# Performance work log

Measured on AMD Instinct MI355X. Metric: run time of the kernel, lower is better.

Reference implementation:

```python
import jax, jax.numpy as jnp
import numpy as np

DIM = 512
NUM_HEADS = 1
WS = 16
B, H, W = 2, WS * WS, 1


def _rel_pos_index(ws):
    # matches Attention.calculate_relative_position_index (no Swin offset -> negatives)
    coords = np.stack(np.meshgrid(np.arange(ws), np.arange(ws), indexing='ij'), 0).reshape(2, -1)
    rel = coords[:, :, None] - coords[:, None, :]          # [2, ws^2, ws^2]
    return rel.transpose(1, 2, 0).sum(-1)                  # [ws^2, ws^2] in [-(2ws-2), 2ws-2]

_NTAB = (2 * WS - 1) ** 2
# torch fancy indexing wraps negative indices; emulate with mod (values are in (-NTAB, NTAB))
_RPI = np.mod(_rel_pos_index(WS), _NTAB).reshape(-1)       # [ws^4]


def setup_inputs() -> dict:
    key = jax.random.key(0)
    ks = jax.random.split(key, 6)
    x = jax.random.normal(ks[0], (B, DIM, H, W), dtype=jnp.float32)
    qkv_w = jax.random.normal(ks[1], (3 * DIM, DIM), dtype=jnp.float32) * (DIM ** -0.5)
    qkv_b = jax.random.normal(ks[2], (3 * DIM,), dtype=jnp.float32) * 0.02
    proj_w = jax.random.normal(ks[3], (DIM, DIM), dtype=jnp.float32) * (DIM ** -0.5)
    proj_b = jax.random.normal(ks[4], (DIM,), dtype=jnp.float32) * 0.02
    rpb = jax.random.normal(ks[5], (_NTAB, NUM_HEADS), dtype=jnp.float32) * 0.02
    return {"x": x, "qkv_w": qkv_w, "qkv_b": qkv_b,
            "proj_w": proj_w, "proj_b": proj_b, "rpb": rpb}


def reference(x, qkv_w, qkv_b, proj_w, proj_b, rpb):
    b, c, h, w = x.shape                                   # [B, C, H, W=1]
    d = c // NUM_HEADS
    scale = d ** -0.5                                      # qk_scale=None -> (dim//nh)^-0.5
    # 1x1 conv == channel matmul
    qkv = jnp.einsum('bchw,oc->bohw', x, qkv_w) + qkv_b[None, :, None, None]
    qkv = qkv.reshape(b, 3, NUM_HEADS, d, h, w)
    q, k, v = qkv[:, 0], qkv[:, 1], qkv[:, 2]              # [B, nh, d, H, W]
    # matmul over last two dims: contracts W -> [B, nh, d, H, H]
    attn = jnp.einsum('bndhw,bndgw->bndhg', q, k) * scale
    idx = jnp.asarray(_RPI)
    bias = rpb[idx].reshape(h * w, h * w, -1).transpose(2, 0, 1)  # [nh, HW, HW] = [1, H, H]
    attn = jax.nn.softmax(attn + bias, axis=-1)
    out = jnp.einsum('bndhg,bndgw->bndhw', attn, v).sum(axis=1)   # sum over heads -> [B, d, H, W]
    out = jnp.einsum('bchw,oc->bohw', out, proj_w) + proj_b[None, :, None, None]
    return out
```

## Files before the change

### kernel.cpp

```cpp
#include <hip/hip_runtime.h>
#include <hip/hip_bf16.h>


#define TOK   256
#define KDIM  512
#define LOG2E 1.4426950408889634f
#define SCALE 0.04419417382415922f

#define EXP2(x) __builtin_amdgcn_exp2f(x)

struct K1Smem {
    union {
        float red[4][6][256];
        float brow[31][258];
    } u;
    float tab2[64];
    float ks_[2][TOK];
    float vs_[2][TOK];
    float qs_[2][TOK];
    float lpart[2][TOK], apart[2][TOK];
};

__global__ __launch_bounds__(256)
void qkv_attn(const float* __restrict__ x, const float* __restrict__ qkv_w,
              const float* __restrict__ qkv_b, const float* __restrict__ rpb,
              float* __restrict__ aout)
{
    __shared__ K1Smem sm;
    const int t    = threadIdx.x;
    const int d0   = blockIdx.x * 2;
    const int b    = blockIdx.y;
    const int w    = t >> 6;
    const int lane = t & 63;

    if (t < 61) {
        const int rel = t - 30;
        sm.tab2[t] = rpb[rel < 0 ? rel + 961 : rel] * LOG2E;
    }

    {
        const float* xb = x + (size_t)b * (KDIM * TOK);
        const int g0 = lane * 4;
        const float* wp[6];
        wp[0] = qkv_w + (size_t)(d0 + 0) * KDIM;
        wp[1] = qkv_w + (size_t)(d0 + 1) * KDIM;
        wp[2] = qkv_w + (size_t)(512 + d0 + 0) * KDIM;
        wp[3] = qkv_w + (size_t)(512 + d0 + 1) * KDIM;
        wp[4] = qkv_w + (size_t)(1024 + d0 + 0) * KDIM;
        wp[5] = qkv_w + (size_t)(1024 + d0 + 1) * KDIM;

        float acc[6][4];
#pragma unroll
        for (int e = 0; e < 6; ++e)
#pragma unroll
            for (int j = 0; j < 4; ++j) acc[e][j] = 0.f;

        const int cbeg = w * 128;
#pragma unroll 1
        for (int c = cbeg; c < cbeg + 128; c += 4) {
            float4 xv[4];
#pragma unroll
            for (int u = 0; u < 4; ++u)
                xv[u] = *(const float4*)(xb + (size_t)(c + u) * TOK + g0);
#pragma unroll
            for (int u = 0; u < 4; ++u) {
#pragma unroll
                for (int e = 0; e < 6; ++e) {
                    const float wv = wp[e][c + u];
                    acc[e][0] = fmaf(wv, xv[u].x, acc[e][0]);
                    acc[e][1] = fmaf(wv, xv[u].y, acc[e][1]);
                    acc[e][2] = fmaf(wv, xv[u].z, acc[e][2]);
                    acc[e][3] = fmaf(wv, xv[u].w, acc[e][3]);
                }
            }
        }
#pragma unroll
        for (int e = 0; e < 6; ++e)
            *(float4*)&sm.u.red[w][e][g0] = make_float4(acc[e][0], acc[e][1],
                                                        acc[e][2], acc[e][3]);
    }
    __syncthreads();

    {
#pragma unroll
        for (int e = 0; e < 6; ++e) {
            const float v = sm.u.red[0][e][t] + sm.u.red[1][e][t] +
                            sm.u.red[2][e][t] + sm.u.red[3][e][t];
            if (e < 2)      sm.qs_[e][t] = v + qkv_b[d0 + e];
            else if (e < 4) sm.ks_[e - 2][t] = (v + qkv_b[512 + d0 + e - 2]) *
                                               (SCALE * LOG2E);
            else            sm.vs_[e - 4][t] = v + qkv_b[1024 + d0 + e - 4];
        }
    }
    __syncthreads();

    {
        const int rg = ((t >> 4) & 15) + (t & 15);
#pragma unroll 1
        for (int it = 0; it < 31; ++it)
            sm.u.brow[it][t] = sm.tab2[it - rg + 30];
    }
    __syncthreads();

    const int dl  = w & 1;
    const int gh  = w >> 1;
    const int qi  = ((lane & 15) << 2) | (lane >> 4);
    const int h0  = qi * 4;
    const int rh0 = (qi >> 2) + 4 * (qi & 3);

    float q[4];
    {
        const float4 q4 = *(const float4*)&sm.qs_[dl][h0];
        q[0] = q4.x; q[1] = q4.y; q[2] = q4.z; q[3] = q4.w;
    }

    float l[4]  = {0.f, 0.f, 0.f, 0.f};
    float am[4] = {0.f, 0.f, 0.f, 0.f};
    const int pbeg = gh * 128;
#pragma unroll 2
    for (int p = pbeg; p < pbeg + 128; p += 4) {
        const float4 k4 = *(const float4*)&sm.ks_[dl][p];
        const float4 v4 = *(const float4*)&sm.vs_[dl][p];
#pragma unroll
        for (int r = 0; r < 4; ++r) {
            const float2 b01 = *(const float2*)&sm.u.brow[rh0 + r][p];
            const float2 b23 = *(const float2*)&sm.u.brow[rh0 + r][p + 2];
            float e;
            e = EXP2(fmaf(q[r], k4.x, b01.x)); l[r] += e; am[r] = fmaf(e, v4.x, am[r]);
            e = EXP2(fmaf(q[r], k4.y, b01.y)); l[r] += e; am[r] = fmaf(e, v4.y, am[r]);
            e = EXP2(fmaf(q[r], k4.z, b23.x)); l[r] += e; am[r] = fmaf(e, v4.z, am[r]);
            e = EXP2(fmaf(q[r], k4.w, b23.y)); l[r] += e; am[r] = fmaf(e, v4.w, am[r]);
        }
    }

    if (gh == 1) {
        *(float4*)&sm.lpart[dl][h0] = make_float4(l[0], l[1], l[2], l[3]);
        *(float4*)&sm.apart[dl][h0] = make_float4(am[0], am[1], am[2], am[3]);
    }
    __syncthreads();
    if (gh == 0) {
        const float4 lo = *(const float4*)&sm.lpart[dl][h0];
        const float4 ao = *(const float4*)&sm.apart[dl][h0];
        float4 o4;
        o4.x = (am[0] + ao.x) / (l[0] + lo.x);
        o4.y = (am[1] + ao.y) / (l[1] + lo.y);
        o4.z = (am[2] + ao.z) / (l[2] + lo.z);
        o4.w = (am[3] + ao.w) / (l[3] + lo.w);
        *(float4*)(aout + ((size_t)b * 512 + d0 + dl) * TOK + h0) = o4;
    }
}

__global__ __launch_bounds__(256)
void proj_fused(const float* __restrict__ aout, const float* __restrict__ proj_w,
                const float* __restrict__ proj_b, float* __restrict__ out)
{
    __shared__ float sred[4][4][256];
    const int t    = threadIdx.x;
    const int o0   = blockIdx.x * 4;
    const int b    = blockIdx.y;
    const int w    = t >> 6;
    const int g0   = (t & 63) * 4;

    const float* ab = aout + (size_t)b * (KDIM * TOK);
    const float* wp[4];
#pragma unroll
    for (int e = 0; e < 4; ++e)
        wp[e] = proj_w + (size_t)(o0 + e) * KDIM;

    float acc[4][4];
#pragma unroll
    for (int e = 0; e < 4; ++e)
#pragma unroll
        for (int j = 0; j < 4; ++j) acc[e][j] = 0.f;

    const int cbeg = w * 128;
#pragma unroll 1
    for (int c = cbeg; c < cbeg + 128; c += 4) {
        float4 av[4];
#pragma unroll
        for (int u = 0; u < 4; ++u)
            av[u] = *(const float4*)(ab + (size_t)(c + u) * TOK + g0);
#pragma unroll
        for (int u = 0; u < 4; ++u) {
#pragma unroll
            for (int e = 0; e < 4; ++e) {
                const float wv = wp[e][c + u];
                acc[e][0] = fmaf(wv, av[u].x, acc[e][0]);
                acc[e][1] = fmaf(wv, av[u].y, acc[e][1]);
                acc[e][2] = fmaf(wv, av[u].z, acc[e][2]);
                acc[e][3] = fmaf(wv, av[u].w, acc[e][3]);
            }
        }
    }
#pragma unroll
    for (int e = 0; e < 4; ++e)
        *(float4*)&sred[w][e][g0] = make_float4(acc[e][0], acc[e][1],
                                                acc[e][2], acc[e][3]);
    __syncthreads();

#pragma unroll
    for (int e = 0; e < 4; ++e) {
        const float v = sred[0][e][t] + sred[1][e][t] +
                        sred[2][e][t] + sred[3][e][t] + proj_b[o0 + e];
        out[((size_t)b * 512 + o0 + e) * TOK + t] = v;
    }
}

extern "C" void kernel_launch(void* const* d_in, const int* in_sizes, int n_in,
                              void* d_out, int out_size, void* d_ws, size_t ws_size,
                              hipStream_t stream)
{
    const float* x      = (const float*)d_in[0];
    const float* qkv_w  = (const float*)d_in[1];
    const float* qkv_b  = (const float*)d_in[2];
    const float* proj_w = (const float*)d_in[3];
    const float* proj_b = (const float*)d_in[4];
    const float* rpb    = (const float*)d_in[5];
    float* out  = (float*)d_out;
    float* aout = (float*)d_ws;

    qkv_attn<<<dim3(256, 2), 256, 0, stream>>>(x, qkv_w, qkv_b, rpb, aout);

    proj_fused<<<dim3(128, 2), 256, 0, stream>>>(aout, proj_w, proj_b, out);
}
```

Before: 110.4 us.

## Widen QKV-attention blocks to four channels and drop materialized bias rows

The QKV kernel now runs 512 threads per block, each block handling four channels, with eight waves splitting the reduction dimension. It uses float4 weight loads and software-prefetches the next x rows. The 31x258 precomputed relative-bias row table is replaced by a 7-entry window read straight from the 61-entry bias table per key group, which removes a shared-memory fill pass and one barrier. The projection kernel gets the same float4 weight loads and x prefetching. The cost is higher register pressure (48 accumulators) and half as many blocks for the QKV kernel.

```diff
diff --git a/kernel.cpp b/kernel.cpp
--- a/kernel.cpp
+++ b/kernel.cpp
@@ -11,102 +11,112 @@
 
 struct K1Smem {
     union {
-        float red[4][6][256];
-        float brow[31][258];
+        float red[8][6][256];
+        struct { float lpart[4][256], apart[4][256]; } mg;
     } u;
-    float tab2[64];
-    float ks_[2][TOK];
-    float vs_[2][TOK];
-    float qs_[2][TOK];
-    float lpart[2][TOK], apart[2][TOK];
+    float stab[64];
+    float qs_[4][256];
+    float ks_[4][256];
+    float vs_[4][256];
 };
 
-__global__ __launch_bounds__(256)
+__global__ __launch_bounds__(512, 2)
 void qkv_attn(const float* __restrict__ x, const float* __restrict__ qkv_w,
               const float* __restrict__ qkv_b, const float* __restrict__ rpb,
               float* __restrict__ aout)
 {
     __shared__ K1Smem sm;
     const int t    = threadIdx.x;
-    const int d0   = blockIdx.x * 2;
-    const int b    = blockIdx.y;
     const int w    = t >> 6;
     const int lane = t & 63;
+    const int d0   = blockIdx.x * 4;
+    const int b    = blockIdx.y;
+    const int g0   = lane * 4;
 
     if (t < 61) {
         const int rel = t - 30;
-        sm.tab2[t] = rpb[rel < 0 ? rel + 961 : rel] * LOG2E;
-    }
-
+        sm.stab[t] = rpb[rel < 0 ? rel + 961 : rel] * LOG2E;
+    }
+
+    float acc[12][4];
+#pragma unroll
+    for (int e = 0; e < 12; ++e)
+#pragma unroll
+        for (int j = 0; j < 4; ++j) acc[e][j] = 0.f;
     {
         const float* xb = x + (size_t)b * (KDIM * TOK);
-        const int g0 = lane * 4;
-        const float* wp[6];
-        wp[0] = qkv_w + (size_t)(d0 + 0) * KDIM;
-        wp[1] = qkv_w + (size_t)(d0 + 1) * KDIM;
-        wp[2] = qkv_w + (size_t)(512 + d0 + 0) * KDIM;
-        wp[3] = qkv_w + (size_t)(512 + d0 + 1) * KDIM;
-        wp[4] = qkv_w + (size_t)(1024 + d0 + 0) * KDIM;
-        wp[5] = qkv_w + (size_t)(1024 + d0 + 1) * KDIM;
-
-        float acc[6][4];
-#pragma unroll
-        for (int e = 0; e < 6; ++e)
-#pragma unroll
-            for (int j = 0; j < 4; ++j) acc[e][j] = 0.f;
-
-        const int cbeg = w * 128;
+        const int cbeg = w * 64;
+        float4 xv[4], xn[4];
+#pragma unroll
+        for (int u = 0; u < 4; ++u)
+            xv[u] = *(const float4*)(xb + (size_t)(cbeg + u) * TOK + g0);
 #pragma unroll 1
-        for (int c = cbeg; c < cbeg + 128; c += 4) {
-            float4 xv[4];
-#pragma unroll
-            for (int u = 0; u < 4; ++u)
-                xv[u] = *(const float4*)(xb + (size_t)(c + u) * TOK + g0);
-#pragma unroll
-            for (int u = 0; u < 4; ++u) {
-#pragma unroll
-                for (int e = 0; e < 6; ++e) {
-                    const float wv = wp[e][c + u];
-                    acc[e][0] = fmaf(wv, xv[u].x, acc[e][0]);
-                    acc[e][1] = fmaf(wv, xv[u].y, acc[e][1]);
-                    acc[e][2] = fmaf(wv, xv[u].z, acc[e][2]);
-                    acc[e][3] = fmaf(wv, xv[u].w, acc[e][3]);
-                }
+        for (int it = 0; it < 16; ++it) {
+            const int c = cbeg + it * 4;
+            if (it < 15) {
+#pragma unroll
+                for (int u = 0; u < 4; ++u)
+                    xn[u] = *(const float4*)(xb + (size_t)(c + 4 + u) * TOK + g0);
             }
-        }
-#pragma unroll
-        for (int e = 0; e < 6; ++e)
-            *(float4*)&sm.u.red[w][e][g0] = make_float4(acc[e][0], acc[e][1],
-                                                        acc[e][2], acc[e][3]);
+#pragma unroll
+            for (int e = 0; e < 12; ++e) {
+                const float4 wv = *(const float4*)(
+                    qkv_w + (size_t)((e >> 2) * 512 + d0 + (e & 3)) * KDIM + c);
+                acc[e][0] = fmaf(wv.x, xv[0].x, acc[e][0]);
+                acc[e][1] = fmaf(wv.x, xv[0].y, acc[e][1]);
+                acc[e][2] = fmaf(wv.x, xv[0].z, acc[e][2]);
+                acc[e][3] = fmaf(wv.x, xv[0].w, acc[e][3]);
+                acc[e][0] = fmaf(wv.y, xv[1].x, acc[e][0]);
+                acc[e][1] = fmaf(wv.y, xv[1].y, acc[e][1]);
+                acc[e][2] = fmaf(wv.y, xv[1].z, acc[e][2]);
+                acc[e][3] = fmaf(wv.y, xv[1].w, acc[e][3]);
+                acc[e][0] = fmaf(wv.z, xv[2].x, acc[e][0]);
+                acc[e][1] = fmaf(wv.z, xv[2].y, acc[e][1]);
+                acc[e][2] = fmaf(wv.z, xv[2].z, acc[e][2]);
+                acc[e][3] = fmaf(wv.z, xv[2].w, acc[e][3]);
+                acc[e][0] = fmaf(wv.w, xv[3].x, acc[e][0]);
+                acc[e][1] = fmaf(wv.w, xv[3].y, acc[e][1]);
+                acc[e][2] = fmaf(wv.w, xv[3].z, acc[e][2]);
+                acc[e][3] = fmaf(wv.w, xv[3].w, acc[e][3]);
+            }
+#pragma unroll
+            for (int u = 0; u < 4; ++u) xv[u] = xn[u];
+        }
+    }
+
+    const int gred = t & 255;
+    const int esub = t >> 8;
+#pragma unroll
+    for (int s = 0; s < 2; ++s) {
+        if (s) __syncthreads();
+#pragma unroll
+        for (int el = 0; el < 6; ++el)
+            *(float4*)&sm.u.red[w][el][g0] =
+                make_float4(acc[s * 6 + el][0], acc[s * 6 + el][1],
+                            acc[s * 6 + el][2], acc[s * 6 + el][3]);
+        __syncthreads();
+#pragma unroll
+        for (int j = 0; j < 3; ++j) {
+            const int el = esub * 3 + j;
+            float sum = 0.f;
+#pragma unroll
+            for (int p = 0; p < 8; ++p) sum += sm.u.red[p][el][gred];
+            const int e = s * 6 + el;
+            const int type = e >> 2, ch = e & 3;
+            if (type == 0)
+                sm.qs_[ch][gred] = sum + qkv_b[d0 + ch];
+            else if (type == 1)
+                sm.ks_[ch][gred] = (sum + qkv_b[512 + d0 + ch]) * (SCALE * LOG2E);
+            else
+                sm.vs_[ch][gred] = sum + qkv_b[1024 + d0 + ch];
+        }
     }
     __syncthreads();
 
-    {
-#pragma unroll
-        for (int e = 0; e < 6; ++e) {
-            const float v = sm.u.red[0][e][t] + sm.u.red[1][e][t] +
-                            sm.u.red[2][e][t] + sm.u.red[3][e][t];
-            if (e < 2)      sm.qs_[e][t] = v + qkv_b[d0 + e];
-            else if (e < 4) sm.ks_[e - 2][t] = (v + qkv_b[512 + d0 + e - 2]) *
-                                               (SCALE * LOG2E);
-            else            sm.vs_[e - 4][t] = v + qkv_b[1024 + d0 + e - 4];
-        }
-    }
-    __syncthreads();
-
-    {
-        const int rg = ((t >> 4) & 15) + (t & 15);
-#pragma unroll 1
-        for (int it = 0; it < 31; ++it)
-            sm.u.brow[it][t] = sm.tab2[it - rg + 30];
-    }
-    __syncthreads();
-
-    const int dl  = w & 1;
-    const int gh  = w >> 1;
-    const int qi  = ((lane & 15) << 2) | (lane >> 4);
-    const int h0  = qi * 4;
-    const int rh0 = (qi >> 2) + 4 * (qi & 3);
+    const int dl  = w & 3;
+    const int gh  = w >> 2;
+    const int h0  = lane * 4;
+    const int rh0 = (lane >> 2) + 4 * (lane & 3);
 
     float q[4];
     {
@@ -121,26 +131,28 @@
     for (int p = pbeg; p < pbeg + 128; p += 4) {
         const float4 k4 = *(const float4*)&sm.ks_[dl][p];
         const float4 v4 = *(const float4*)&sm.vs_[dl][p];
+        const int i0 = rh0 + 30 - ((p >> 4) + (p & 15));
+        float f[7];
+#pragma unroll
+        for (int k = 0; k < 7; ++k) f[k] = sm.stab[i0 - 3 + k];
 #pragma unroll
         for (int r = 0; r < 4; ++r) {
-            const float2 b01 = *(const float2*)&sm.u.brow[rh0 + r][p];
-            const float2 b23 = *(const float2*)&sm.u.brow[rh0 + r][p + 2];
             float e;
-            e = EXP2(fmaf(q[r], k4.x, b01.x)); l[r] += e; am[r] = fmaf(e, v4.x, am[r]);
-            e = EXP2(fmaf(q[r], k4.y, b01.y)); l[r] += e; am[r] = fmaf(e, v4.y, am[r]);
-            e = EXP2(fmaf(q[r], k4.z, b23.x)); l[r] += e; am[r] = fmaf(e, v4.z, am[r]);
-            e = EXP2(fmaf(q[r], k4.w, b23.y)); l[r] += e; am[r] = fmaf(e, v4.w, am[r]);
+            e = EXP2(fmaf(q[r], k4.x, f[3 + r])); l[r] += e; am[r] = fmaf(e, v4.x, am[r]);
+            e = EXP2(fmaf(q[r], k4.y, f[2 + r])); l[r] += e; am[r] = fmaf(e, v4.y, am[r]);
+            e = EXP2(fmaf(q[r], k4.z, f[1 + r])); l[r] += e; am[r] = fmaf(e, v4.z, am[r]);
+            e = EXP2(fmaf(q[r], k4.w, f[0 + r])); l[r] += e; am[r] = fmaf(e, v4.w, am[r]);
         }
     }
 
     if (gh == 1) {
-        *(float4*)&sm.lpart[dl][h0] = make_float4(l[0], l[1], l[2], l[3]);
-        *(float4*)&sm.apart[dl][h0] = make_float4(am[0], am[1], am[2], am[3]);
+        *(float4*)&sm.u.mg.lpart[dl][h0] = make_float4(l[0], l[1], l[2], l[3]);
+        *(float4*)&sm.u.mg.apart[dl][h0] = make_float4(am[0], am[1], am[2], am[3]);
     }
     __syncthreads();
     if (gh == 0) {
-        const float4 lo = *(const float4*)&sm.lpart[dl][h0];
-        const float4 ao = *(const float4*)&sm.apart[dl][h0];
+        const float4 lo = *(const float4*)&sm.u.mg.lpart[dl][h0];
+        const float4 ao = *(const float4*)&sm.u.mg.apart[dl][h0];
         float4 o4;
         o4.x = (am[0] + ao.x) / (l[0] + lo.x);
         o4.y = (am[1] + ao.y) / (l[1] + lo.y);
@@ -155,42 +167,55 @@
                 const float* __restrict__ proj_b, float* __restrict__ out)
 {
     __shared__ float sred[4][4][256];
-    const int t    = threadIdx.x;
-    const int o0   = blockIdx.x * 4;
-    const int b    = blockIdx.y;
-    const int w    = t >> 6;
-    const int g0   = (t & 63) * 4;
+    const int t  = threadIdx.x;
+    const int o0 = blockIdx.x * 4;
+    const int b  = blockIdx.y;
+    const int w  = t >> 6;
+    const int g0 = (t & 63) * 4;
 
     const float* ab = aout + (size_t)b * (KDIM * TOK);
-    const float* wp[4];
+
+    float acc[4][4];
 #pragma unroll
     for (int e = 0; e < 4; ++e)
-        wp[e] = proj_w + (size_t)(o0 + e) * KDIM;
-
-    float acc[4][4];
-#pragma unroll
-    for (int e = 0; e < 4; ++e)
 #pragma unroll
         for (int j = 0; j < 4; ++j) acc[e][j] = 0.f;
 
     const int cbeg = w * 128;
+    float4 av[4], an[4];
+#pragma unroll
+    for (int u = 0; u < 4; ++u)
+        av[u] = *(const float4*)(ab + (size_t)(cbeg + u) * TOK + g0);
 #pragma unroll 1
-    for (int c = cbeg; c < cbeg + 128; c += 4) {
-        float4 av[4];
-#pragma unroll
-        for (int u = 0; u < 4; ++u)
-            av[u] = *(const float4*)(ab + (size_t)(c + u) * TOK + g0);
-#pragma unroll
-        for (int u = 0; u < 4; ++u) {
-#pragma unroll
-            for (int e = 0; e < 4; ++e) {
-                const float wv = wp[e][c + u];
-                acc[e][0] = fmaf(wv, av[u].x, acc[e][0]);
-                acc[e][1] = fmaf(wv, av[u].y, acc[e][1]);
-                acc[e][2] = fmaf(wv, av[u].z, acc[e][2]);
-                acc[e][3] = fmaf(wv, av[u].w, acc[e][3]);
-            }
-        }
+    for (int it = 0; it < 32; ++it) {
+        const int c = cbeg + it * 4;
+        if (it < 31) {
+#pragma unroll
+            for (int u = 0; u < 4; ++u)
+                an[u] = *(const float4*)(ab + (size_t)(c + 4 + u) * TOK + g0);
+        }
+#pragma unroll
+        for (int e = 0; e < 4; ++e) {
+            const float4 wv = *(const float4*)(proj_w + (size_t)(o0 + e) * KDIM + c);
+            acc[e][0] = fmaf(wv.x, av[0].x, acc[e][0]);
+            acc[e][1] = fmaf(wv.x, av[0].y, acc[e][1]);
+            acc[e][2] = fmaf(wv.x, av[0].z, acc[e][2]);
+            acc[e][3] = fmaf(wv.x, av[0].w, acc[e][3]);
+            acc[e][0] = fmaf(wv.y, av[1].x, acc[e][0]);
+            acc[e][1] = fmaf(wv.y, av[1].y, acc[e][1]);
+            acc[e][2] = fmaf(wv.y, av[1].z, acc[e][2]);
+            acc[e][3] = fmaf(wv.y, av[1].w, acc[e][3]);
+            acc[e][0] = fmaf(wv.z, av[2].x, acc[e][0]);
+            acc[e][1] = fmaf(wv.z, av[2].y, acc[e][1]);
+            acc[e][2] = fmaf(wv.z, av[2].z, acc[e][2]);
+            acc[e][3] = fmaf(wv.z, av[2].w, acc[e][3]);
+            acc[e][0] = fmaf(wv.w, av[3].x, acc[e][0]);
+            acc[e][1] = fmaf(wv.w, av[3].y, acc[e][1]);
+            acc[e][2] = fmaf(wv.w, av[3].z, acc[e][2]);
+            acc[e][3] = fmaf(wv.w, av[3].w, acc[e][3]);
+        }
+#pragma unroll
+        for (int u = 0; u < 4; ++u) av[u] = an[u];
     }
 #pragma unroll
     for (int e = 0; e < 4; ++e)
@@ -219,7 +244,7 @@
     float* out  = (float*)d_out;
     float* aout = (float*)d_ws;
 
-    qkv_attn<<<dim3(256, 2), 256, 0, stream>>>(x, qkv_w, qkv_b, rpb, aout);
+    qkv_attn<<<dim3(128, 2), 512, 0, stream>>>(x, qkv_w, qkv_b, rpb, aout);
 
     proj_fused<<<dim3(128, 2), 256, 0, stream>>>(aout, proj_w, proj_b, out);
 }
```

Result: slower. 122.2 us (+10.8%).

## Drop split-K reductions in matmuls and compute rel-pos bias from small table

Applied to the files above, without the earlier changes.

Both channel matmuls now give each thread one token and the full 512-channel reduction, with register double-buffered prefetch of x rows. This removes the shared-memory partial-sum reduction and its barriers. The attention loop now reads the relative-position bias from a 61-entry table using the Toeplitz structure, replacing the materialized 31x258 bias rows and their build pass. The cost is longer serial FMA chains per thread and less reuse of each loaded x element, since one thread now handles one token instead of four.

```diff
diff --git a/kernel.cpp b/kernel.cpp
--- a/kernel.cpp
+++ b/kernel.cpp
@@ -10,14 +10,10 @@
 #define EXP2(x) __builtin_amdgcn_exp2f(x)
 
 struct K1Smem {
-    union {
-        float red[4][6][256];
-        float brow[31][258];
-    } u;
-    float tab2[64];
+    float stab[64];
+    float qs_[2][TOK];
     float ks_[2][TOK];
     float vs_[2][TOK];
-    float qs_[2][TOK];
     float lpart[2][TOK], apart[2][TOK];
 };
 
@@ -28,19 +24,19 @@
 {
     __shared__ K1Smem sm;
     const int t    = threadIdx.x;
+    const int w    = t >> 6;
+    const int lane = t & 63;
     const int d0   = blockIdx.x * 2;
     const int b    = blockIdx.y;
-    const int w    = t >> 6;
-    const int lane = t & 63;
+    const int g    = w * 64 + lane;
 
     if (t < 61) {
         const int rel = t - 30;
-        sm.tab2[t] = rpb[rel < 0 ? rel + 961 : rel] * LOG2E;
+        sm.stab[t] = rpb[rel < 0 ? rel + 961 : rel] * LOG2E;
     }
 
     {
-        const float* xb = x + (size_t)b * (KDIM * TOK);
-        const int g0 = lane * 4;
+        const float* xb = x + (size_t)b * (KDIM * TOK) + g;
         const float* wp[6];
         wp[0] = qkv_w + (size_t)(d0 + 0) * KDIM;
         wp[1] = qkv_w + (size_t)(d0 + 1) * KDIM;
@@ -49,64 +45,41 @@
         wp[4] = qkv_w + (size_t)(1024 + d0 + 0) * KDIM;
         wp[5] = qkv_w + (size_t)(1024 + d0 + 1) * KDIM;
 
-        float acc[6][4];
+        float acc[6] = {0.f, 0.f, 0.f, 0.f, 0.f, 0.f};
+        float xv[8], xn[8];
 #pragma unroll
-        for (int e = 0; e < 6; ++e)
+        for (int u = 0; u < 8; ++u) xv[u] = xb[(size_t)u * TOK];
+#pragma unroll 1
+        for (int it = 0; it < 64; ++it) {
+            const int cb = it * 8;
+            if (it < 63) {
 #pragma unroll
-            for (int j = 0; j < 4; ++j) acc[e][j] = 0.f;
-
-        const int cbeg = w * 128;
-#pragma unroll 1
-        for (int c = cbeg; c < cbeg + 128; c += 4) {
-            float4 xv[4];
+                for (int u = 0; u < 8; ++u)
+                    xn[u] = xb[(size_t)(cb + 8 + u) * TOK];
+            }
 #pragma unroll
-            for (int u = 0; u < 4; ++u)
-                xv[u] = *(const float4*)(xb + (size_t)(c + u) * TOK + g0);
+            for (int u = 0; u < 8; ++u) {
+                const int c = cb + u;
 #pragma unroll
-            for (int u = 0; u < 4; ++u) {
+                for (int e = 0; e < 6; ++e)
+                    acc[e] = fmaf(wp[e][c], xv[u], acc[e]);
+            }
 #pragma unroll
-                for (int e = 0; e < 6; ++e) {
-                    const float wv = wp[e][c + u];
-                    acc[e][0] = fmaf(wv, xv[u].x, acc[e][0]);
-                    acc[e][1] = fmaf(wv, xv[u].y, acc[e][1]);
-                    acc[e][2] = fmaf(wv, xv[u].z, acc[e][2]);
-                    acc[e][3] = fmaf(wv, xv[u].w, acc[e][3]);
-                }
-            }
+            for (int u = 0; u < 8; ++u) xv[u] = xn[u];
         }
-#pragma unroll
-        for (int e = 0; e < 6; ++e)
-            *(float4*)&sm.u.red[w][e][g0] = make_float4(acc[e][0], acc[e][1],
-                                                        acc[e][2], acc[e][3]);
-    }
-    __syncthreads();
-
-    {
-#pragma unroll
-        for (int e = 0; e < 6; ++e) {
-            const float v = sm.u.red[0][e][t] + sm.u.red[1][e][t] +
-                            sm.u.red[2][e][t] + sm.u.red[3][e][t];
-            if (e < 2)      sm.qs_[e][t] = v + qkv_b[d0 + e];
-            else if (e < 4) sm.ks_[e - 2][t] = (v + qkv_b[512 + d0 + e - 2]) *
-                                               (SCALE * LOG2E);
-            else            sm.vs_[e - 4][t] = v + qkv_b[1024 + d0 + e - 4];
-        }
-    }
-    __syncthreads();
-
-    {
-        const int rg = ((t >> 4) & 15) + (t & 15);
-#pragma unroll 1
-        for (int it = 0; it < 31; ++it)
-            sm.u.brow[it][t] = sm.tab2[it - rg + 30];
+        sm.qs_[0][g] = acc[0] + qkv_b[d0 + 0];
+        sm.qs_[1][g] = acc[1] + qkv_b[d0 + 1];
+        sm.ks_[0][g] = (acc[2] + qkv_b[512 + d0 + 0]) * (SCALE * LOG2E);
+        sm.ks_[1][g] = (acc[3] + qkv_b[512 + d0 + 1]) * (SCALE * LOG2E);
+        sm.vs_[0][g] = acc[4] + qkv_b[1024 + d0 + 0];
+        sm.vs_[1][g] = acc[5] + qkv_b[1024 + d0 + 1];
     }
     __syncthreads();
 
     const int dl  = w & 1;
     const int gh  = w >> 1;
-    const int qi  = ((lane & 15) << 2) | (lane >> 4);
-    const int h0  = qi * 4;
-    const int rh0 = (qi >> 2) + 4 * (qi & 3);
+    const int h0  = lane * 4;
+    const int rh0 = (lane >> 2) + 4 * (lane & 3);
 
     float q[4];
     {
@@ -121,15 +94,17 @@
     for (int p = pbeg; p < pbeg + 128; p += 4) {
         const float4 k4 = *(const float4*)&sm.ks_[dl][p];
         const float4 v4 = *(const float4*)&sm.vs_[dl][p];
+        const int i0 = rh0 + 30 - ((p >> 4) + (p & 15));
+        float f[7];
+#pragma unroll
+        for (int k = 0; k < 7; ++k) f[k] = sm.stab[i0 - 3 + k];
 #pragma unroll
         for (int r = 0; r < 4; ++r) {
-            const float2 b01 = *(const float2*)&sm.u.brow[rh0 + r][p];
-            const float2 b23 = *(const float2*)&sm.u.brow[rh0 + r][p + 2];
             float e;
-            e = EXP2(fmaf(q[r], k4.x, b01.x)); l[r] += e; am[r] = fmaf(e, v4.x, am[r]);
-            e = EXP2(fmaf(q[r], k4.y, b01.y)); l[r] += e; am[r] = fmaf(e, v4.y, am[r]);
-            e = EXP2(fmaf(q[r], k4.z, b23.x)); l[r] += e; am[r] = fmaf(e, v4.z, am[r]);
-            e = EXP2(fmaf(q[r], k4.w, b23.y)); l[r] += e; am[r] = fmaf(e, v4.w, am[r]);
+            e = EXP2(fmaf(q[r], k4.x, f[3 + r])); l[r] += e; am[r] = fmaf(e, v4.x, am[r]);
+            e = EXP2(fmaf(q[r], k4.y, f[2 + r])); l[r] += e; am[r] = fmaf(e, v4.y, am[r]);
+            e = EXP2(fmaf(q[r], k4.z, f[1 + r])); l[r] += e; am[r] = fmaf(e, v4.z, am[r]);
+            e = EXP2(fmaf(q[r], k4.w, f[0 + r])); l[r] += e; am[r] = fmaf(e, v4.w, am[r]);
         }
     }
 
@@ -154,56 +129,45 @@
 void proj_fused(const float* __restrict__ aout, const float* __restrict__ proj_w,
                 const float* __restrict__ proj_b, float* __restrict__ out)
 {
-    __shared__ float sred[4][4][256];
     const int t    = threadIdx.x;
+    const int w    = t >> 6;
+    const int lane = t & 63;
     const int o0   = blockIdx.x * 4;
     const int b    = blockIdx.y;
-    const int w    = t >> 6;
-    const int g0   = (t & 63) * 4;
+    const int g    = w * 64 + lane;
 
-    const float* ab = aout + (size_t)b * (KDIM * TOK);
+    const float* ab = aout + (size_t)b * (KDIM * TOK) + g;
     const float* wp[4];
 #pragma unroll
     for (int e = 0; e < 4; ++e)
         wp[e] = proj_w + (size_t)(o0 + e) * KDIM;
 
-    float acc[4][4];
+    float acc[4] = {0.f, 0.f, 0.f, 0.f};
+    float av[8], an[8];
+#pragma unroll
+    for (int u = 0; u < 8; ++u) av[u] = ab[(size_t)u * TOK];
+#pragma unroll 1
+    for (int it = 0; it < 64; ++it) {
+        const int cb = it * 8;
+        if (it < 63) {
+#pragma unroll
+            for (int u = 0; u < 8; ++u)
+                an[u] = ab[(size_t)(cb + 8 + u) * TOK];
+        }
+#pragma unroll
+        for (int u = 0; u < 8; ++u) {
+            const int c = cb + u;
+#pragma unroll
+            for (int e = 0; e < 4; ++e)
+                acc[e] = fmaf(wp[e][c], av[u], acc[e]);
+        }
+#pragma unroll
+        for (int u = 0; u < 8; ++u) av[u] = an[u];
+    }
+
 #pragma unroll
     for (int e = 0; e < 4; ++e)
-#pragma unroll
-        for (int j = 0; j < 4; ++j) acc[e][j] = 0.f;
-
-    const int cbeg = w * 128;
-#pragma unroll 1
-    for (int c = cbeg; c < cbeg + 128; c += 4) {
-        float4 av[4];
-#pragma unroll
-        for (int u = 0; u < 4; ++u)
-            av[u] = *(const float4*)(ab + (size_t)(c + u) * TOK + g0);
-#pragma unroll
-        for (int u = 0; u < 4; ++u) {
-#pragma unroll
-            for (int e = 0; e < 4; ++e) {
-                const float wv = wp[e][c + u];
-                acc[e][0] = fmaf(wv, av[u].x, acc[e][0]);
-                acc[e][1] = fmaf(wv, av[u].y, acc[e][1]);
-                acc[e][2] = fmaf(wv, av[u].z, acc[e][2]);
-                acc[e][3] = fmaf(wv, av[u].w, acc[e][3]);
-            }
-        }
-    }
-#pragma unroll
-    for (int e = 0; e < 4; ++e)
-        *(float4*)&sred[w][e][g0] = make_float4(acc[e][0], acc[e][1],
-                                                acc[e][2], acc[e][3]);
-    __syncthreads();
-
-#pragma unroll
-    for (int e = 0; e < 4; ++e) {
-        const float v = sred[0][e][t] + sred[1][e][t] +
-                        sred[2][e][t] + sred[3][e][t] + proj_b[o0 + e];
-        out[((size_t)b * 512 + o0 + e) * TOK + t] = v;
-    }
+        out[((size_t)b * 512 + o0 + e) * TOK + g] = acc[e] + proj_b[o0 + e];
 }
 
 extern "C" void kernel_launch(void* const* d_in, const int* in_sizes, int n_in,
```

Result: slower. 144.1 us (+30.6%).
